# Performance work log

Hardware: AMD Instinct MI355X
Metric: run time of the kernel (lower is better)

## Reference

```python
import jax, jax.numpy as jnp
import numpy as np

# TTCReward hyperparameters (init_kwargs)
LONG_TH = 0.0
LAT_TH = 0.0
H = 4               # num_historical_intervals
LEAST_MIN_TTC = 0.95
DT = 0.5            # time_span_per_interval

NUM_EGO = 32        # scenes (len(ptr) - 1)
AGENTS_PER = 128
N_AGENTS = NUM_EGO * AGENTS_PER   # 4096
T_TOTAL = 34


def setup_inputs():
    key = jax.random.key(0)
    k1, k2, k3, k4 = jax.random.split(key, 4)
    infer_position = jax.random.uniform(k1, (N_AGENTS, T_TOTAL, 2), jnp.float32) * 100.0
    infer_heading = (jax.random.uniform(k2, (N_AGENTS, T_TOTAL), jnp.float32) - 0.5) * (2.0 * np.pi)
    box = jax.random.uniform(k3, (N_AGENTS, 4), jnp.float32) * 1.5 + 0.5  # front/rear/left/right extents
    infer_valid_mask = jax.random.uniform(k4, (N_AGENTS, T_TOTAL)) > 0.05
    batch = jnp.repeat(jnp.arange(NUM_EGO, dtype=jnp.int32), AGENTS_PER)
    ptr = jnp.arange(NUM_EGO + 1, dtype=jnp.int32) * AGENTS_PER
    return dict(infer_position=infer_position, infer_heading=infer_heading, box=box,
                infer_valid_mask=infer_valid_mask, batch=batch, ptr=ptr)


def _corners(pos, yaw, box):
    # pos [N,T,2], yaw [N,T], box [N,4] = (front, rear, left, right) extents
    f, r, l, rt = box[:, 0], box[:, 1], box[:, 2], box[:, 3]
    local = jnp.stack([jnp.stack([f, l], -1), jnp.stack([f, -rt], -1),
                       jnp.stack([-r, -rt], -1), jnp.stack([-r, l], -1)], axis=1)  # [N,4,2]
    c = jnp.cos(yaw)[:, :, None]
    s = jnp.sin(yaw)[:, :, None]
    lx = local[:, None, :, 0]
    ly = local[:, None, :, 1]
    x = lx * c - ly * s + pos[:, :, None, 0]
    y = lx * s + ly * c + pos[:, :, None, 1]
    return jnp.stack([x, y], -1)  # [N,T,4,2]


def _loss(lx, ly, bf, br, bl, brt):
    # min over 4 box-side clamped penetrations, then max over the 4 corners (last axis)
    long_t = jnp.minimum(jnp.maximum(bf + LONG_TH - lx, 0.0),
                         jnp.maximum(br + LONG_TH + lx, 0.0))
    lat_t = jnp.minimum(jnp.maximum(bl + LAT_TH - ly, 0.0),
                        jnp.maximum(brt + LAT_TH + ly, 0.0))
    return jnp.max(jnp.minimum(long_t, lat_t), axis=-1)


def reference(infer_position, infer_heading, box, infer_valid_mask, batch, ptr):
    N = infer_heading.shape[0]
    vel = (infer_position[:, H:] - infer_position[:, H - 1:-1]) / DT
    pos = infer_position[:, H:] + vel * LEAST_MIN_TTC           # [N,T,2] position at min-TTC horizon
    yaw = infer_heading[:, H:]                                  # [N,T]
    corner = _corners(pos, yaw, box)                            # [N,T,4,2]

    ego = ptr[:-1]                                              # [B]
    B = ego.shape[0]
    Tn = pos.shape[1]

    ego_pos = jnp.swapaxes(pos[ego], 0, 1)                      # [T,B,2]
    ego_yaw = jnp.swapaxes(yaw[ego], 0, 1)                      # [T,B]
    ego_corner = jnp.swapaxes(corner[ego], 0, 1)                # [T,B,4,2]
    ego_box = box[ego]                                          # [B,4]
    agent_pos = jnp.swapaxes(pos, 0, 1)                         # [T,N,2]
    agent_yaw = jnp.swapaxes(yaw, 0, 1)                         # [T,N]
    agent_corner = jnp.swapaxes(corner, 0, 1)                   # [T,N,4,2]

    valid = infer_valid_mask[:, H:]                             # [N,T]
    edge_mask = (valid[ego].T[:, :, None] & valid.T[:, None, :]
                 & (batch[ego][:, None] == batch[None, :])[None]
                 & (ego[:, None] != jnp.arange(N)[None, :])[None])  # [T,B,N]

    # ego corners expressed in each agent's local frame, vs agent box
    d = ego_corner[:, :, None] - agent_pos[:, None, :, None]   # [T,B,N,4,2]
    ca = jnp.cos(agent_yaw)[:, None, :, None]
    sa = jnp.sin(agent_yaw)[:, None, :, None]
    ego_in_agent = _loss(d[..., 0] * ca + d[..., 1] * sa,
                         -d[..., 0] * sa + d[..., 1] * ca,
                         box[:, 0][None, None, :, None], box[:, 1][None, None, :, None],
                         box[:, 2][None, None, :, None], box[:, 3][None, None, :, None])  # [T,B,N]

    # agent corners expressed in each ego's local frame, vs ego box
    d2 = agent_corner[:, None] - ego_pos[:, :, None, None]     # [T,B,N,4,2]
    ce = jnp.cos(ego_yaw)[:, :, None, None]
    se = jnp.sin(ego_yaw)[:, :, None, None]
    agent_in_ego = _loss(d2[..., 0] * ce + d2[..., 1] * se,
                         -d2[..., 0] * se + d2[..., 1] * ce,
                         ego_box[:, 0][None, :, None, None], ego_box[:, 1][None, :, None, None],
                         ego_box[:, 2][None, :, None, None], ego_box[:, 3][None, :, None, None])  # [T,B,N]

    # Replicate original dense_to_sparse edge orderings: ego_in_agent edges enumerate
    # edge_mask in (t,i,j) order; agent_in_ego edges use the transposed (t,j,i) order.
    # The torch code max-combines the two lists per *position* e before scatter_max
    # over rows t*B+i (taken from the (t,i,j) ordering), which we reproduce exactly
    # via rank-based scatters into fixed-size [E] buffers.
    E = Tn * B * N
    rows = jnp.broadcast_to((jnp.arange(Tn)[:, None] * B + jnp.arange(B)[None, :])[:, :, None],
                            (Tn, B, N)).reshape(-1)
    m = edge_mask.reshape(-1)
    idx = jnp.where(m, jnp.cumsum(m.astype(jnp.int32)) - 1, E)      # OOB index E -> dropped
    mT = jnp.swapaxes(edge_mask, 1, 2).reshape(-1)
    idxT = jnp.where(mT, jnp.cumsum(mT.astype(jnp.int32)) - 1, E)
    neg_inf = jnp.float32(-jnp.inf)
    b_by_rank = jnp.full((E,), neg_inf).at[idx].set(ego_in_agent.reshape(-1))
    a_by_rank = jnp.full((E,), neg_inf).at[idxT].set(jnp.swapaxes(agent_in_ego, 1, 2).reshape(-1))
    rows_by_rank = jnp.zeros((E,), jnp.int32).at[idx].set(rows.astype(jnp.int32))
    ttc_loss = jnp.maximum(a_by_rank, b_by_rank)
    seg_max = jax.ops.segment_max(ttc_loss, rows_by_rank, num_segments=Tn * B)  # empty -> -inf
    # reward per ego: all timesteps have max ttc_loss <= 0 (no edge -> -inf -> True)
    return jnp.all((seg_max <= 0.0).reshape(Tn, B), axis=0).astype(jnp.float32)
```

## Files before the change

kernel.cpp:

```cpp
#include <hip/hip_runtime.h>
#include <math.h>

#define NUM_EGO   32
#define AGENTS_PER 128
#define T_TOTAL   34
#define H_OFF     4
#define TN        30
#define SCALE     1.9f

__global__ void ttc_init_out(float* __restrict__ out) {
    int i = threadIdx.x;
    if (i < NUM_EGO) out[i] = 1.0f;
}

__global__ __launch_bounds__(AGENTS_PER) void ttc_main(
    const float* __restrict__ posg,
    const float* __restrict__ headg,
    const float* __restrict__ boxg,
    const int*   __restrict__ validg,
    const int*   __restrict__ ptrg,
    float* __restrict__ out)
{
    const int blk = blockIdx.x;
    const int b   = blk / TN;
    const int t   = blk % TN;
    const int tt  = t + H_OFF;

    __shared__ float s_ego[16];
    __shared__ int   s_evalid;
    __shared__ int   s_any;
    __shared__ int   s_e0, s_e1;

    if (threadIdx.x == 0) {
        int e0 = ptrg[b];
        int e1 = ptrg[b + 1];
        s_e0 = e0; s_e1 = e1;
        s_any = 0;
        const int e = e0;
        s_evalid = validg[e * T_TOTAL + tt];
        float px1 = posg[(e * T_TOTAL + tt) * 2 + 0];
        float py1 = posg[(e * T_TOTAL + tt) * 2 + 1];
        float px0 = posg[(e * T_TOTAL + tt - 1) * 2 + 0];
        float py0 = posg[(e * T_TOTAL + tt - 1) * 2 + 1];
        float ex = px1 + SCALE * (px1 - px0);
        float ey = py1 + SCALE * (py1 - py0);
        float yaw = headg[e * T_TOTAL + tt];
        float c = cosf(yaw), s = sinf(yaw);
        float f  = boxg[e * 4 + 0];
        float r  = boxg[e * 4 + 1];
        float l  = boxg[e * 4 + 2];
        float rt = boxg[e * 4 + 3];
        s_ego[0] = ex; s_ego[1] = ey; s_ego[2] = c; s_ego[3] = s;
        float lxs[4] = { f,  f, -r, -r };
        float lys[4] = { l, -rt, -rt,  l };
        #pragma unroll
        for (int k = 0; k < 4; ++k) {
            s_ego[4 + 2 * k] = lxs[k] * c - lys[k] * s + ex;
            s_ego[5 + 2 * k] = lxs[k] * s + lys[k] * c + ey;
        }
        s_ego[12] = f; s_ego[13] = r; s_ego[14] = l; s_ego[15] = rt;
    }
    __syncthreads();

    if (!s_evalid) return;

    const int e0 = s_e0, e1 = s_e1;
    const int n = e0 + threadIdx.x;

    float loss = 0.0f;
    if (n < e1 && n != e0 && validg[n * T_TOTAL + tt] != 0) {
        float px1 = posg[(n * T_TOTAL + tt) * 2 + 0];
        float py1 = posg[(n * T_TOTAL + tt) * 2 + 1];
        float px0 = posg[(n * T_TOTAL + tt - 1) * 2 + 0];
        float py0 = posg[(n * T_TOTAL + tt - 1) * 2 + 1];
        float ax = px1 + SCALE * (px1 - px0);
        float ay = py1 + SCALE * (py1 - py0);
        float ayaw = headg[n * T_TOTAL + tt];
        float ca = cosf(ayaw), sa = sinf(ayaw);
        float af  = boxg[n * 4 + 0];
        float ar  = boxg[n * 4 + 1];
        float al  = boxg[n * 4 + 2];
        float art = boxg[n * 4 + 3];

        const float ex = s_ego[0], ey = s_ego[1];
        const float ce = s_ego[2], se = s_ego[3];
        const float ef = s_ego[12], er = s_ego[13], el = s_ego[14], ert = s_ego[15];

        float L1 = 0.0f;
        #pragma unroll
        for (int k = 0; k < 4; ++k) {
            float dx = s_ego[4 + 2 * k] - ax;
            float dy = s_ego[5 + 2 * k] - ay;
            float lx =  dx * ca + dy * sa;
            float ly = -dx * sa + dy * ca;
            float lo = fminf(fmaxf(af - lx, 0.0f), fmaxf(ar + lx, 0.0f));
            float la = fminf(fmaxf(al - ly, 0.0f), fmaxf(art + ly, 0.0f));
            L1 = fmaxf(L1, fminf(lo, la));
        }

        float lxs[4] = { af,  af, -ar, -ar };
        float lys[4] = { al, -art, -art,  al };
        float L2 = 0.0f;
        #pragma unroll
        for (int k = 0; k < 4; ++k) {
            float cxw = lxs[k] * ca - lys[k] * sa + ax;
            float cyw = lxs[k] * sa + lys[k] * ca + ay;
            float dx = cxw - ex;
            float dy = cyw - ey;
            float lx =  dx * ce + dy * se;
            float ly = -dx * se + dy * ce;
            float lo = fminf(fmaxf(ef - lx, 0.0f), fmaxf(er + lx, 0.0f));
            float la = fminf(fmaxf(el - ly, 0.0f), fmaxf(ert + ly, 0.0f));
            L2 = fmaxf(L2, fminf(lo, la));
        }

        loss = fmaxf(L1, L2);
    }

    if (loss > 0.0f) s_any = 1;
    __syncthreads();
    if (threadIdx.x == 0 && s_any) {
        out[b] = 0.0f;
    }
}

extern "C" void kernel_launch(void* const* d_in, const int* in_sizes, int n_in,
                              void* d_out, int out_size, void* d_ws, size_t ws_size,
                              hipStream_t stream) {
    const float* posg   = (const float*)d_in[0];
    const float* headg  = (const float*)d_in[1];
    const float* boxg   = (const float*)d_in[2];
    const int*   validg = (const int*)  d_in[3];
    const int*   ptrg   = (const int*)  d_in[5];
    float* out = (float*)d_out;

    ttc_init_out<<<1, 64, 0, stream>>>(out);
    ttc_main<<<NUM_EGO * TN, AGENTS_PER, 0, stream>>>(posg, headg, boxg, validg, ptrg, out);
}
```

Baseline: 68.68 us.

## Fuse init and main kernels into one block per scene looping over timesteps

New measurement: 92.07 us. 34.1% more time.

```diff
diff --git a/kernel.cpp b/kernel.cpp
--- a/kernel.cpp
+++ b/kernel.cpp
@@ -1,19 +1,14 @@
 #include <hip/hip_runtime.h>
 #include <math.h>
 
-#define NUM_EGO   32
+#define NUM_EGO    32
 #define AGENTS_PER 128
-#define T_TOTAL   34
-#define H_OFF     4
-#define TN        30
-#define SCALE     1.9f
+#define T_TOTAL    34
+#define H_OFF      4
+#define TN         30
+#define SCALE      1.9f
 
-__global__ void ttc_init_out(float* __restrict__ out) {
-    int i = threadIdx.x;
-    if (i < NUM_EGO) out[i] = 1.0f;
-}
-
-__global__ __launch_bounds__(AGENTS_PER) void ttc_main(
+__global__ __launch_bounds__(AGENTS_PER) void ttc_fused(
     const float* __restrict__ posg,
     const float* __restrict__ headg,
     const float* __restrict__ boxg,
@@ -21,76 +16,94 @@
     const int*   __restrict__ ptrg,
     float* __restrict__ out)
 {
-    const int blk = blockIdx.x;
-    const int b   = blk / TN;
-    const int t   = blk % TN;
-    const int tt  = t + H_OFF;
+    const int b = blockIdx.x;
 
-    __shared__ float s_ego[16];
-    __shared__ int   s_evalid;
+    __shared__ float s_ex[TN], s_ey[TN], s_ce[TN], s_se[TN];
+    __shared__ float s_cx[TN][4], s_cy[TN][4];
+    __shared__ int   s_evalid[TN];
+    __shared__ float s_ebox[4];
+    __shared__ int   s_e0;
     __shared__ int   s_any;
-    __shared__ int   s_e0, s_e1;
 
     if (threadIdx.x == 0) {
+        s_any = 0;
         int e0 = ptrg[b];
-        int e1 = ptrg[b + 1];
-        s_e0 = e0; s_e1 = e1;
-        s_any = 0;
-        const int e = e0;
-        s_evalid = validg[e * T_TOTAL + tt];
-        float px1 = posg[(e * T_TOTAL + tt) * 2 + 0];
-        float py1 = posg[(e * T_TOTAL + tt) * 2 + 1];
-        float px0 = posg[(e * T_TOTAL + tt - 1) * 2 + 0];
-        float py0 = posg[(e * T_TOTAL + tt - 1) * 2 + 1];
+        s_e0 = e0;
+        s_ebox[0] = boxg[e0 * 4 + 0];
+        s_ebox[1] = boxg[e0 * 4 + 1];
+        s_ebox[2] = boxg[e0 * 4 + 2];
+        s_ebox[3] = boxg[e0 * 4 + 3];
+    }
+    __syncthreads();
+
+    const int e0 = s_e0;
+
+    if (threadIdx.x < TN) {
+        const int t  = threadIdx.x;
+        const int tt = t + H_OFF;
+        s_evalid[t] = validg[e0 * T_TOTAL + tt];
+        float px1 = posg[(e0 * T_TOTAL + tt) * 2 + 0];
+        float py1 = posg[(e0 * T_TOTAL + tt) * 2 + 1];
+        float px0 = posg[(e0 * T_TOTAL + tt - 1) * 2 + 0];
+        float py0 = posg[(e0 * T_TOTAL + tt - 1) * 2 + 1];
         float ex = px1 + SCALE * (px1 - px0);
         float ey = py1 + SCALE * (py1 - py0);
-        float yaw = headg[e * T_TOTAL + tt];
+        float yaw = headg[e0 * T_TOTAL + tt];
         float c = cosf(yaw), s = sinf(yaw);
-        float f  = boxg[e * 4 + 0];
-        float r  = boxg[e * 4 + 1];
-        float l  = boxg[e * 4 + 2];
-        float rt = boxg[e * 4 + 3];
-        s_ego[0] = ex; s_ego[1] = ey; s_ego[2] = c; s_ego[3] = s;
+        s_ex[t] = ex; s_ey[t] = ey; s_ce[t] = c; s_se[t] = s;
+        float f  = s_ebox[0];
+        float r  = s_ebox[1];
+        float l  = s_ebox[2];
+        float rt = s_ebox[3];
         float lxs[4] = { f,  f, -r, -r };
         float lys[4] = { l, -rt, -rt,  l };
         #pragma unroll
         for (int k = 0; k < 4; ++k) {
-            s_ego[4 + 2 * k] = lxs[k] * c - lys[k] * s + ex;
-            s_ego[5 + 2 * k] = lxs[k] * s + lys[k] * c + ey;
+            s_cx[t][k] = lxs[k] * c - lys[k] * s + ex;
+            s_cy[t][k] = lxs[k] * s + lys[k] * c + ey;
         }
-        s_ego[12] = f; s_ego[13] = r; s_ego[14] = l; s_ego[15] = rt;
     }
     __syncthreads();
 
-    if (!s_evalid) return;
+    const int n = e0 + threadIdx.x;
+    const bool is_ego = (threadIdx.x == 0);
 
-    const int e0 = s_e0, e1 = s_e1;
-    const int n = e0 + threadIdx.x;
+    const float af  = boxg[n * 4 + 0];
+    const float ar  = boxg[n * 4 + 1];
+    const float al  = boxg[n * 4 + 2];
+    const float art = boxg[n * 4 + 3];
+    const float ef  = s_ebox[0], er = s_ebox[1], el = s_ebox[2], ert = s_ebox[3];
 
-    float loss = 0.0f;
-    if (n < e1 && n != e0 && validg[n * T_TOTAL + tt] != 0) {
+    const float lxs[4] = { af,  af, -ar, -ar };
+    const float lys[4] = { al, -art, -art,  al };
+
+    bool any = false;
+
+    float ppx = posg[(n * T_TOTAL + H_OFF - 1) * 2 + 0];
+    float ppy = posg[(n * T_TOTAL + H_OFF - 1) * 2 + 1];
+
+    for (int t = 0; t < TN; ++t) {
+        const int tt = t + H_OFF;
         float px1 = posg[(n * T_TOTAL + tt) * 2 + 0];
         float py1 = posg[(n * T_TOTAL + tt) * 2 + 1];
-        float px0 = posg[(n * T_TOTAL + tt - 1) * 2 + 0];
-        float py0 = posg[(n * T_TOTAL + tt - 1) * 2 + 1];
-        float ax = px1 + SCALE * (px1 - px0);
-        float ay = py1 + SCALE * (py1 - py0);
+        float ax = px1 + SCALE * (px1 - ppx);
+        float ay = py1 + SCALE * (py1 - ppy);
+        ppx = px1; ppy = py1;
+
+        if (is_ego || !s_evalid[t]) continue;
+        if (validg[n * T_TOTAL + tt] == 0) continue;
+
         float ayaw = headg[n * T_TOTAL + tt];
         float ca = cosf(ayaw), sa = sinf(ayaw);
-        float af  = boxg[n * 4 + 0];
-        float ar  = boxg[n * 4 + 1];
-        float al  = boxg[n * 4 + 2];
-        float art = boxg[n * 4 + 3];
 
-        const float ex = s_ego[0], ey = s_ego[1];
-        const float ce = s_ego[2], se = s_ego[3];
-        const float ef = s_ego[12], er = s_ego[13], el = s_ego[14], ert = s_ego[15];
+        const float ex = s_ex[t], ey = s_ey[t];
+        const float ce = s_ce[t], se = s_se[t];
 
         float L1 = 0.0f;
         #pragma unroll
         for (int k = 0; k < 4; ++k) {
-            float dx = s_ego[4 + 2 * k] - ax;
-            float dy = s_ego[5 + 2 * k] - ay;
+            float dx = s_cx[t][k] - ax;
+            float dy = s_cy[t][k] - ay;
             float lx =  dx * ca + dy * sa;
             float ly = -dx * sa + dy * ca;
             float lo = fminf(fmaxf(af - lx, 0.0f), fmaxf(ar + lx, 0.0f));
@@ -98,8 +111,6 @@
             L1 = fmaxf(L1, fminf(lo, la));
         }
 
-        float lxs[4] = { af,  af, -ar, -ar };
-        float lys[4] = { al, -art, -art,  al };
         float L2 = 0.0f;
         #pragma unroll
         for (int k = 0; k < 4; ++k) {
@@ -114,13 +125,13 @@
             L2 = fmaxf(L2, fminf(lo, la));
         }
 
-        loss = fmaxf(L1, L2);
+        any |= (fmaxf(L1, L2) > 0.0f);
     }
 
-    if (loss > 0.0f) s_any = 1;
+    if (any) s_any = 1;
     __syncthreads();
-    if (threadIdx.x == 0 && s_any) {
-        out[b] = 0.0f;
+    if (threadIdx.x == 0) {
+        out[b] = s_any ? 0.0f : 1.0f;
     }
 }
 
@@ -134,6 +145,5 @@
     const int*   ptrg   = (const int*)  d_in[5];
     float* out = (float*)d_out;
 
-    ttc_init_out<<<1, 64, 0, stream>>>(out);
-    ttc_main<<<NUM_EGO * TN, AGENTS_PER, 0, stream>>>(posg, headg, boxg, validg, ptrg, out);
+    ttc_fused<<<NUM_EGO, AGENTS_PER, 0, stream>>>(posg, headg, boxg, validg, ptrg, out);
 }
```

## Drop shared-memory ego staging and barriers; compute ego per thread, memset init

Applied to the files above, without the earlier changes.

Measured after the change: 66.76 us. -2.8%, faster.

```diff
diff --git a/kernel.cpp b/kernel.cpp
--- a/kernel.cpp
+++ b/kernel.cpp
@@ -1,17 +1,12 @@
 #include <hip/hip_runtime.h>
 #include <math.h>
 
-#define NUM_EGO   32
+#define NUM_EGO    32
 #define AGENTS_PER 128
-#define T_TOTAL   34
-#define H_OFF     4
-#define TN        30
-#define SCALE     1.9f
-
-__global__ void ttc_init_out(float* __restrict__ out) {
-    int i = threadIdx.x;
-    if (i < NUM_EGO) out[i] = 1.0f;
-}
+#define T_TOTAL    34
+#define H_OFF      4
+#define TN         30
+#define SCALE      1.9f
 
 __global__ __launch_bounds__(AGENTS_PER) void ttc_main(
     const float* __restrict__ posg,
@@ -25,101 +20,68 @@
     const int b   = blk / TN;
     const int t   = blk % TN;
     const int tt  = t + H_OFF;
+    const int a   = threadIdx.x;
 
-    __shared__ float s_ego[16];
-    __shared__ int   s_evalid;
-    __shared__ int   s_any;
-    __shared__ int   s_e0, s_e1;
+    const int e0 = ptrg[b];
+    const int n  = e0 + a;
 
-    if (threadIdx.x == 0) {
-        int e0 = ptrg[b];
-        int e1 = ptrg[b + 1];
-        s_e0 = e0; s_e1 = e1;
-        s_any = 0;
-        const int e = e0;
-        s_evalid = validg[e * T_TOTAL + tt];
-        float px1 = posg[(e * T_TOTAL + tt) * 2 + 0];
-        float py1 = posg[(e * T_TOTAL + tt) * 2 + 1];
-        float px0 = posg[(e * T_TOTAL + tt - 1) * 2 + 0];
-        float py0 = posg[(e * T_TOTAL + tt - 1) * 2 + 1];
-        float ex = px1 + SCALE * (px1 - px0);
-        float ey = py1 + SCALE * (py1 - py0);
-        float yaw = headg[e * T_TOTAL + tt];
-        float c = cosf(yaw), s = sinf(yaw);
-        float f  = boxg[e * 4 + 0];
-        float r  = boxg[e * 4 + 1];
-        float l  = boxg[e * 4 + 2];
-        float rt = boxg[e * 4 + 3];
-        s_ego[0] = ex; s_ego[1] = ey; s_ego[2] = c; s_ego[3] = s;
-        float lxs[4] = { f,  f, -r, -r };
-        float lys[4] = { l, -rt, -rt,  l };
-        #pragma unroll
-        for (int k = 0; k < 4; ++k) {
-            s_ego[4 + 2 * k] = lxs[k] * c - lys[k] * s + ex;
-            s_ego[5 + 2 * k] = lxs[k] * s + lys[k] * c + ey;
-        }
-        s_ego[12] = f; s_ego[13] = r; s_ego[14] = l; s_ego[15] = rt;
-    }
-    __syncthreads();
+    const int   ev   = validg[e0 * T_TOTAL + tt];
+    const float2 ep1 = *(const float2*)&posg[(e0 * T_TOTAL + tt) * 2];
+    const float2 ep0 = *(const float2*)&posg[(e0 * T_TOTAL + tt - 1) * 2];
+    const float eyaw = headg[e0 * T_TOTAL + tt];
+    const float4 ebx = *(const float4*)&boxg[e0 * 4];
+    const int   av   = validg[n * T_TOTAL + tt];
+    const float2 ap1 = *(const float2*)&posg[(n * T_TOTAL + tt) * 2];
+    const float2 ap0 = *(const float2*)&posg[(n * T_TOTAL + tt - 1) * 2];
+    const float ayaw = headg[n * T_TOTAL + tt];
+    const float4 abx = *(const float4*)&boxg[n * 4];
 
-    if (!s_evalid) return;
+    const float ex = ep1.x + SCALE * (ep1.x - ep0.x);
+    const float ey = ep1.y + SCALE * (ep1.y - ep0.y);
+    const float ax = ap1.x + SCALE * (ap1.x - ap0.x);
+    const float ay = ap1.y + SCALE * (ap1.y - ap0.y);
+    const float ce = __cosf(eyaw), se = __sinf(eyaw);
+    const float ca = __cosf(ayaw), sa = __sinf(ayaw);
 
-    const int e0 = s_e0, e1 = s_e1;
-    const int n = e0 + threadIdx.x;
+    const float ef = ebx.x, er = ebx.y, el = ebx.z, ert = ebx.w;
+    const float af = abx.x, ar = abx.y, al = abx.z, art = abx.w;
 
-    float loss = 0.0f;
-    if (n < e1 && n != e0 && validg[n * T_TOTAL + tt] != 0) {
-        float px1 = posg[(n * T_TOTAL + tt) * 2 + 0];
-        float py1 = posg[(n * T_TOTAL + tt) * 2 + 1];
-        float px0 = posg[(n * T_TOTAL + tt - 1) * 2 + 0];
-        float py0 = posg[(n * T_TOTAL + tt - 1) * 2 + 1];
-        float ax = px1 + SCALE * (px1 - px0);
-        float ay = py1 + SCALE * (py1 - py0);
-        float ayaw = headg[n * T_TOTAL + tt];
-        float ca = cosf(ayaw), sa = sinf(ayaw);
-        float af  = boxg[n * 4 + 0];
-        float ar  = boxg[n * 4 + 1];
-        float al  = boxg[n * 4 + 2];
-        float art = boxg[n * 4 + 3];
+    const float elx[4] = { ef,  ef, -er, -er };
+    const float ely[4] = { el, -ert, -ert,  el };
+    const float alx[4] = { af,  af, -ar, -ar };
+    const float aly[4] = { al, -art, -art,  al };
 
-        const float ex = s_ego[0], ey = s_ego[1];
-        const float ce = s_ego[2], se = s_ego[3];
-        const float ef = s_ego[12], er = s_ego[13], el = s_ego[14], ert = s_ego[15];
-
-        float L1 = 0.0f;
-        #pragma unroll
-        for (int k = 0; k < 4; ++k) {
-            float dx = s_ego[4 + 2 * k] - ax;
-            float dy = s_ego[5 + 2 * k] - ay;
-            float lx =  dx * ca + dy * sa;
-            float ly = -dx * sa + dy * ca;
-            float lo = fminf(fmaxf(af - lx, 0.0f), fmaxf(ar + lx, 0.0f));
-            float la = fminf(fmaxf(al - ly, 0.0f), fmaxf(art + ly, 0.0f));
-            L1 = fmaxf(L1, fminf(lo, la));
-        }
-
-        float lxs[4] = { af,  af, -ar, -ar };
-        float lys[4] = { al, -art, -art,  al };
-        float L2 = 0.0f;
-        #pragma unroll
-        for (int k = 0; k < 4; ++k) {
-            float cxw = lxs[k] * ca - lys[k] * sa + ax;
-            float cyw = lxs[k] * sa + lys[k] * ca + ay;
-            float dx = cxw - ex;
-            float dy = cyw - ey;
-            float lx =  dx * ce + dy * se;
-            float ly = -dx * se + dy * ce;
-            float lo = fminf(fmaxf(ef - lx, 0.0f), fmaxf(er + lx, 0.0f));
-            float la = fminf(fmaxf(el - ly, 0.0f), fmaxf(ert + ly, 0.0f));
-            L2 = fmaxf(L2, fminf(lo, la));
-        }
-
-        loss = fmaxf(L1, L2);
+    float L1 = 0.0f;
+    #pragma unroll
+    for (int k = 0; k < 4; ++k) {
+        float cxw = elx[k] * ce - ely[k] * se + ex;
+        float cyw = elx[k] * se + ely[k] * ce + ey;
+        float dx = cxw - ax;
+        float dy = cyw - ay;
+        float lx =  dx * ca + dy * sa;
+        float ly = -dx * sa + dy * ca;
+        float lo = fminf(fmaxf(af - lx, 0.0f), fmaxf(ar + lx, 0.0f));
+        float la = fminf(fmaxf(al - ly, 0.0f), fmaxf(art + ly, 0.0f));
+        L1 = fmaxf(L1, fminf(lo, la));
     }
 
-    if (loss > 0.0f) s_any = 1;
-    __syncthreads();
-    if (threadIdx.x == 0 && s_any) {
+    float L2 = 0.0f;
+    #pragma unroll
+    for (int k = 0; k < 4; ++k) {
+        float cxw = alx[k] * ca - aly[k] * sa + ax;
+        float cyw = alx[k] * sa + aly[k] * ca + ay;
+        float dx = cxw - ex;
+        float dy = cyw - ey;
+        float lx =  dx * ce + dy * se;
+        float ly = -dx * se + dy * ce;
+        float lo = fminf(fmaxf(ef - lx, 0.0f), fmaxf(er + lx, 0.0f));
+        float la = fminf(fmaxf(el - ly, 0.0f), fmaxf(ert + ly, 0.0f));
+        L2 = fmaxf(L2, fminf(lo, la));
+    }
+
+    const bool hit = (a != 0) & (ev != 0) & (av != 0) &
+                     (fmaxf(L1, L2) > 0.0f);
+    if (hit) {
         out[b] = 0.0f;
     }
 }
@@ -134,6 +96,7 @@
     const int*   ptrg   = (const int*)  d_in[5];
     float* out = (float*)d_out;
 
-    ttc_init_out<<<1, 64, 0, stream>>>(out);
-    ttc_main<<<NUM_EGO * TN, AGENTS_PER, 0, stream>>>(posg, headg, boxg, validg, ptrg, out);
+    hipMemsetD32Async((hipDeviceptr_t)out, 0x3F800000, NUM_EGO, stream);
+    ttc_main<<<NUM_EGO * TN, AGENTS_PER, 0, stream>>>(
+        posg, headg, boxg, validg, ptrg, out);
 }
```
